# Performance work log

Hardware: AMD Instinct MI355X
Metric: run time of the kernel (lower is better)

Reference implementation:

```python
import jax, jax.numpy as jnp
import numpy as np

N = 100000
E = 1600000
D_IN = 128
D_OUT = 128
HEADS = 4
C = D_OUT // HEADS  # per-head channels = 32
NEG_SLOPE = 0.2
EPS_SOFTMAX = 1e-16
EPS_LN = 1e-5


def setup_inputs() -> dict:
    key = jax.random.key(0)
    ks = jax.random.split(key, 10)
    x = jax.random.normal(ks[0], (N, D_IN), dtype=jnp.float32)
    edge_index = jax.random.randint(ks[1], (2, E), 0, N, dtype=jnp.int64)
    s = 1.0 / np.sqrt(D_IN)
    W = jax.random.normal(ks[2], (D_IN, HEADS * C), dtype=jnp.float32) * s
    att_src = jax.random.normal(ks[3], (HEADS, C), dtype=jnp.float32) * (1.0 / np.sqrt(C))
    att_dst = jax.random.normal(ks[4], (HEADS, C), dtype=jnp.float32) * (1.0 / np.sqrt(C))
    gat_bias = jax.random.normal(ks[5], (D_OUT,), dtype=jnp.float32) * 0.02
    skip_W = jax.random.normal(ks[6], (D_IN, D_OUT), dtype=jnp.float32) * s
    skip_b = jax.random.normal(ks[7], (D_OUT,), dtype=jnp.float32) * 0.02
    ln_g = jnp.ones((D_OUT,), dtype=jnp.float32)
    ln_b = jnp.zeros((D_OUT,), dtype=jnp.float32)
    return {"x": x, "edge_index": edge_index, "W": W, "att_src": att_src,
            "att_dst": att_dst, "gat_bias": gat_bias, "skip_W": skip_W,
            "skip_b": skip_b, "ln_g": ln_g, "ln_b": ln_b}


def _gat_edge_conv(x, src, dst, W, att_src, att_dst, gat_bias, skip_W, skip_b, ln_g, ln_b):
    n = x.shape[0]
    h = (x @ W).reshape(n, HEADS, C)                      # [N,H,C]
    a_s = jnp.einsum('nhc,hc->nh', h, att_src)            # [N,H]
    a_d = jnp.einsum('nhc,hc->nh', h, att_dst)            # [N,H]
    e = jax.nn.leaky_relu(a_s[src] + a_d[dst], NEG_SLOPE)  # [E,H]
    # segment softmax over incoming edges of each dst node
    m = jax.ops.segment_max(e, dst, num_segments=n)        # [N,H]
    p = jnp.exp(e - m[dst])
    z = jax.ops.segment_sum(p, dst, num_segments=n)        # [N,H]
    alpha = p / (z[dst] + EPS_SOFTMAX)                     # [E,H]
    msg = h[src] * alpha[:, :, None]                       # [E,H,C]
    out = jax.ops.segment_sum(msg, dst, num_segments=n)    # [N,H,C]
    out = out.reshape(n, HEADS * C) + gat_bias
    out = out + x @ skip_W + skip_b
    mu = out.mean(-1, keepdims=True)
    var = ((out - mu) ** 2).mean(-1, keepdims=True)
    return (out - mu) * jax.lax.rsqrt(var + EPS_LN) * ln_g + ln_b


def reference(x, edge_index, W, att_src, att_dst, gat_bias, skip_W, skip_b, ln_g, ln_b):
    n = x.shape[0]
    loops = jnp.arange(n, dtype=edge_index.dtype)          # PyG GATConv add_self_loops=True
    src = jnp.concatenate([edge_index[0], loops])
    dst = jnp.concatenate([edge_index[1], loops])
    return _gat_edge_conv(x, src, dst, W, att_src, att_dst, gat_bias, skip_W, skip_b, ln_g, ln_b)
```

## Files before the change

### kernel.cpp

```cpp
#include <hip/hip_runtime.h>
#include <hip/hip_bf16.h>

#define D 128
#define HEADS 4
#define NEG_SLOPE 0.2f
#define QSCALE 0.0625f
#define QUNSCALE 16.0f

#define BCAP64 1280
#define NB_HIST 1600
#define BEPT 16
#define BCHUNK (256 * BEPT)
#define WPREP_BLOCKS 128
#define LDSPAD 136

typedef __attribute__((ext_vector_type(8))) short short8;
typedef __attribute__((ext_vector_type(4))) float f32x4;
typedef __attribute__((ext_vector_type(2))) float f32x2;
typedef __attribute__((ext_vector_type(2))) _Float16 h2;

__device__ __forceinline__ float lrelu(float v) {
    return fmaxf(v, NEG_SLOPE * v);
}

__device__ __forceinline__ short f2bf(float v) {
    __hip_bfloat16 b = __float2bfloat16(v);
    short s;
    __builtin_memcpy(&s, &b, 2);
    return s;
}

__device__ __forceinline__ unsigned short f2h(float v) {
    _Float16 h = (_Float16)v;
    unsigned short s;
    __builtin_memcpy(&s, &h, 2);
    return s;
}

__global__ __launch_bounds__(256)
void prep_kernel(const float* __restrict__ W, const float* __restrict__ S,
                 short* __restrict__ wsT,
                 const int* __restrict__ ei, int* __restrict__ woffA,
                 unsigned int* __restrict__ pairs, int E_, int nb64, int BA) {
    const int t = threadIdx.x;
    if ((int)blockIdx.x >= BA) {
        const int idx = (blockIdx.x - BA) * 256 + t;
        const int nn = idx >> 7, k = idx & 127;
        const float v = (nn < 128) ? W[k * D + nn] : S[k * D + (nn - 128)];
        wsT[idx] = f2bf(v);
        return;
    }
    __shared__ int hist[NB_HIST];
    __shared__ int gbase[NB_HIST];
    for (int q = t; q < nb64; q += 256) hist[q] = 0;
    __syncthreads();
    int sv[BEPT], dv[BEPT], rk[BEPT];
    const int base = blockIdx.x * BCHUNK;
    #pragma unroll
    for (int i = 0; i < BEPT; ++i) {
        const int e = base + i * 256 + t;
        if (e < E_) {
            sv[i] = ei[e];
            dv[i] = ei[E_ + e];
            rk[i] = atomicAdd(&hist[dv[i] >> 6], 1);
        } else {
            sv[i] = -1;
        }
    }
    __syncthreads();
    for (int q = t; q < nb64; q += 256) {
        const int v = hist[q];
        gbase[q] = v ? (q * BCAP64 + atomicAdd(&woffA[q], v)) : 0;
    }
    __syncthreads();
    #pragma unroll
    for (int i = 0; i < BEPT; ++i) {
        if (sv[i] >= 0) {
            const int q = dv[i] >> 6;
            const unsigned int pos = (unsigned int)(gbase[q] + rk[i]);
            if (pos < (unsigned int)(q + 1) * BCAP64)
                pairs[pos] = ((unsigned int)sv[i] << 6) | (unsigned int)(dv[i] & 63);
        }
    }
}

__global__ __launch_bounds__(512, 4)
void mid_kernel(const float* __restrict__ x, const short* __restrict__ wsT,
                const float* __restrict__ skip_b, const float* __restrict__ gat_bias,
                const float* __restrict__ att_src, const float* __restrict__ att_dst,
                unsigned short* __restrict__ hb, unsigned short* __restrict__ baseb,
                float* __restrict__ a_s, float* __restrict__ a_d,
                const unsigned int* __restrict__ pairs, const int* __restrict__ wcur,
                int* __restrict__ cnt, int* __restrict__ offs, int* __restrict__ ssrc,
                int n, int nb64, int nbbB) {
    __shared__ __align__(16) char smem[64 * LDSPAD * 2];
    const int t = threadIdx.x;
    if ((int)blockIdx.x < nbbB) {
        int* lds = (int*)smem;
        const int sub = t >> 8, tt = t & 255;
        int* nh = lds + sub * 160;
        int* sc = lds + sub * 160 + 80;
        const int qb = blockIdx.x * 2 + sub;
        const bool valid = qb < nb64;
        const int sbeg = valid ? qb * BCAP64 : 0;
        int total = valid ? wcur[qb] : 0;
        if (total > BCAP64) total = BCAP64;
        const int send = sbeg + total;
        if (tt < 64) nh[tt] = 0;
        __syncthreads();
        unsigned int pk[6];
        int rk[6];
        int nl = 0;
        #pragma unroll
        for (int r = 0; r < 5; ++r) {
            const int e = sbeg + r * 256 + tt;
            if (e < send) {
                const unsigned int p = pairs[e];
                const int rr = atomicAdd(&nh[p & 63], 1);
                pk[nl] = p; rk[nl] = rr; ++nl;
            }
        }
        __syncthreads();
        const int v = (tt < 64) ? nh[tt] : 0;
        if (tt < 64) sc[tt] = v;
        __syncthreads();
        for (int off = 1; off < 64; off <<= 1) {
            const int xv = (tt >= off && tt < 64) ? sc[tt - off] : 0;
            __syncthreads();
            if (tt < 64) sc[tt] += xv;
            __syncthreads();
        }
        const int ex = (tt < 64) ? sc[tt] - v : 0;
        if (tt < 64 && valid) {
            const int node = qb * 64 + tt;
            if (node < n) { cnt[node] = v; offs[node] = sbeg + ex; }
        }
        __syncthreads();
        if (tt < 64) nh[tt] = ex;
        __syncthreads();
        for (int i = 0; i < nl; ++i)
            ssrc[sbeg + nh[pk[i] & 63] + rk[i]] = (int)(pk[i] >> 6);
        return;
    }
    short (*xs)[LDSPAD] = (short(*)[LDSPAD])smem;
    const int row0 = (blockIdx.x - nbbB) * 64;
    #pragma unroll
    for (int i = 0; i < 4; ++i) {
        const int f = t + 512 * i;
        const int row = f >> 5, c4 = (f & 31) * 4;
        float4 v = make_float4(0.f, 0.f, 0.f, 0.f);
        if (row0 + row < n) v = *(const float4*)&x[(size_t)(row0 + row) * D + c4];
        short4 s4;
        s4.x = f2bf(v.x); s4.y = f2bf(v.y); s4.z = f2bf(v.z); s4.w = f2bf(v.w);
        *(short4*)&xs[row][c4] = s4;
    }
    __syncthreads();
    const int wv = t >> 6, lane = t & 63;
    const int lo = lane & 15, hi = lane >> 4;
    const int wr = wv >> 2;
    const int wc = wv & 3;
    f32x4 acc[2][4] = {};
    #pragma unroll
    for (int k0 = 0; k0 < 128; k0 += 32) {
        const int kk = k0 + hi * 8;
        short8 a0 = *(const short8*)&xs[wr * 32 + lo][kk];
        short8 a1 = *(const short8*)&xs[wr * 32 + 16 + lo][kk];
        #pragma unroll
        for (int nt = 0; nt < 4; ++nt) {
            short8 b = *(const short8*)&wsT[(wc * 64 + nt * 16 + lo) * D + kk];
            acc[0][nt] = __builtin_amdgcn_mfma_f32_16x16x32_bf16(a0, b, acc[0][nt], 0, 0, 0);
            acc[1][nt] = __builtin_amdgcn_mfma_f32_16x16x32_bf16(a1, b, acc[1][nt], 0, 0, 0);
        }
    }
    if (wc < 2) {
        float as_[4], ad_[4];
        #pragma unroll
        for (int nt = 0; nt < 4; ++nt) {
            const int c = wc * 64 + nt * 16 + lo;
            as_[nt] = att_src[c];
            ad_[nt] = att_dst[c];
        }
        #pragma unroll
        for (int mt = 0; mt < 2; ++mt) {
            #pragma unroll
            for (int reg = 0; reg < 4; ++reg) {
                float ps0 = acc[mt][0][reg] * as_[0] + acc[mt][1][reg] * as_[1];
                float ps1 = acc[mt][2][reg] * as_[2] + acc[mt][3][reg] * as_[3];
                float pd0 = acc[mt][0][reg] * ad_[0] + acc[mt][1][reg] * ad_[1];
                float pd1 = acc[mt][2][reg] * ad_[2] + acc[mt][3][reg] * ad_[3];
                #pragma unroll
                for (int off = 1; off < 16; off <<= 1) {
                    ps0 += __shfl_xor(ps0, off, 64);
                    ps1 += __shfl_xor(ps1, off, 64);
                    pd0 += __shfl_xor(pd0, off, 64);
                    pd1 += __shfl_xor(pd1, off, 64);
                }
                if (lo == 0) {
                    const int r = row0 + wr * 32 + mt * 16 + hi * 4 + reg;
                    if (r < n) {
                        a_s[r * HEADS + wc * 2 + 0] = ps0;
                        a_s[r * HEADS + wc * 2 + 1] = ps1;
                        a_d[r * HEADS + wc * 2 + 0] = pd0;
                        a_d[r * HEADS + wc * 2 + 1] = pd1;
                    }
                }
            }
        }
    }
    #pragma unroll
    for (int nt = 0; nt < 4; ++nt) {
        const int cc = wc * 64 + nt * 16 + lo;
        const bool isH = cc < 128;
        const float bb = isH ? 0.f : (skip_b[cc - 128] + gat_bias[cc - 128]);
        unsigned short* dst = isH ? hb : baseb;
        const int c = isH ? cc : cc - 128;
        #pragma unroll
        for (int mt = 0; mt < 2; ++mt) {
            const int rbase = row0 + wr * 32 + mt * 16 + hi * 4;
            #pragma unroll
            for (int reg = 0; reg < 4; ++reg) {
                const int r = rbase + reg;
                if (r < n) dst[(size_t)r * D + c] = f2h(acc[mt][nt][reg] + bb);
            }
        }
    }
}

__global__ __launch_bounds__(256)
void gather_kernel(const int* __restrict__ offs, const int* __restrict__ cnt,
                   const int* __restrict__ ssrc, const float* __restrict__ a_s,
                   const float* __restrict__ a_d, const uint4* __restrict__ hb16,
                   const uint4* __restrict__ baseb16,
                   const float* __restrict__ ln_g, const float* __restrict__ ln_b,
                   float* __restrict__ out, int n) {
    const int lane = threadIdx.x & 63;
    const int i = blockIdx.x * 4 + (threadIdx.x >> 6);
    if (i >= n) return;
    const int e4 = lane >> 2, h4 = lane & 3;
    const int l15 = lane & 15;
    const int grp = lane >> 4;
    const int hh = l15 >> 2;
    const uint4 bv = baseb16[(size_t)i * 16 + l15];
    const float2 g2 = ((const float2*)ln_g)[l15 * 4 + grp];
    const float2 lb2 = ((const float2*)ln_b)[l15 * 4 + grp];
    const float as_h4 = a_s[i * HEADS + h4];
    const float ad_h4 = a_d[i * HEADS + h4];
    const float qself = __expf(lrelu(as_h4 + ad_h4));
    float zacc = (e4 == 0) ? qself : 0.f;
    h2 acc0 = {0.f, 0.f}, acc1 = {0.f, 0.f}, acc2 = {0.f, 0.f}, acc3 = {0.f, 0.f};
    {
        const float qs = __shfl(qself, hh, 64) * QSCALE;
        if (grp == 0) {
            const uint4 u = hb16[(size_t)i * 16 + l15];
            const _Float16 wh = (_Float16)qs;
            const h2 w2 = {wh, wh};
            acc0 = __builtin_bit_cast(h2, u.x) * w2;
            acc1 = __builtin_bit_cast(h2, u.y) * w2;
            acc2 = __builtin_bit_cast(h2, u.z) * w2;
            acc3 = __builtin_bit_cast(h2, u.w) * w2;
        }
    }
    const int o = offs[i];
    const int c = cnt[i];
    for (int k0 = 0; k0 < c; k0 += 16) {
        const int rem = c - k0;
        int srow = 0;
        float q = 0.f;
        if (e4 < rem) {
            const int sidx = ssrc[o + k0 + e4];
            srow = sidx << 4;
            q = __expf(lrelu(a_s[sidx * HEADS + h4] + ad_h4));
        }
        zacc += q;
        const _Float16 qh = (_Float16)(q * QSCALE);
        const h2 qv = {qh, qh};
        const int qpk = __builtin_bit_cast(int, qv);
        const int m = rem < 16 ? rem : 16;
        int ee = 0;
        for (; ee + 8 <= m; ee += 8) {
            const int slA = (ee + grp) << 2;
            const int slB = (ee + 4 + grp) << 2;
            const int rA = __shfl(srow, slA, 64) + l15;
            const int rB = __shfl(srow, slB, 64) + l15;
            const h2 qA = __builtin_bit_cast(h2, __shfl(qpk, slA + hh, 64));
            const h2 qB = __builtin_bit_cast(h2, __shfl(qpk, slB + hh, 64));
            const uint4 uA = hb16[(size_t)(unsigned)rA];
            const uint4 uB = hb16[(size_t)(unsigned)rB];
            acc0 += __builtin_bit_cast(h2, uA.x) * qA;
            acc1 += __builtin_bit_cast(h2, uA.y) * qA;
            acc2 += __builtin_bit_cast(h2, uA.z) * qA;
            acc3 += __builtin_bit_cast(h2, uA.w) * qA;
            acc0 += __builtin_bit_cast(h2, uB.x) * qB;
            acc1 += __builtin_bit_cast(h2, uB.y) * qB;
            acc2 += __builtin_bit_cast(h2, uB.z) * qB;
            acc3 += __builtin_bit_cast(h2, uB.w) * qB;
        }
        for (; ee < m; ee += 4) {
            const int slot = ee + grp;
            const int sl = slot << 2;
            const int rA = __shfl(srow, sl, 64) + l15;
            const h2 qA = __builtin_bit_cast(h2, __shfl(qpk, sl + hh, 64));
            if (slot < m) {
                const uint4 uA = hb16[(size_t)(unsigned)rA];
                acc0 += __builtin_bit_cast(h2, uA.x) * qA;
                acc1 += __builtin_bit_cast(h2, uA.y) * qA;
                acc2 += __builtin_bit_cast(h2, uA.z) * qA;
                acc3 += __builtin_bit_cast(h2, uA.w) * qA;
            }
        }
    }
    #pragma unroll
    for (int off = 16; off < 64; off <<= 1) {
        acc0 += __builtin_bit_cast(h2, __shfl_xor(__builtin_bit_cast(int, acc0), off, 64));
        acc1 += __builtin_bit_cast(h2, __shfl_xor(__builtin_bit_cast(int, acc1), off, 64));
        acc2 += __builtin_bit_cast(h2, __shfl_xor(__builtin_bit_cast(int, acc2), off, 64));
        acc3 += __builtin_bit_cast(h2, __shfl_xor(__builtin_bit_cast(int, acc3), off, 64));
    }
    #pragma unroll
    for (int off = 4; off < 64; off <<= 1) zacc += __shfl_xor(zacc, off, 64);
    const float zz = __shfl(zacc, hh, 64);
    const float rz = QUNSCALE / (zz + 1e-16f);
    const h2 b0 = __builtin_bit_cast(h2, bv.x);
    const h2 b1 = __builtin_bit_cast(h2, bv.y);
    const h2 b2 = __builtin_bit_cast(h2, bv.z);
    const h2 b3 = __builtin_bit_cast(h2, bv.w);
    const float v0 = (float)acc0.x * rz + (float)b0.x;
    const float v1 = (float)acc0.y * rz + (float)b0.y;
    const float v2 = (float)acc1.x * rz + (float)b1.x;
    const float v3 = (float)acc1.y * rz + (float)b1.y;
    const float v4 = (float)acc2.x * rz + (float)b2.x;
    const float v5 = (float)acc2.y * rz + (float)b2.y;
    const float v6 = (float)acc3.x * rz + (float)b3.x;
    const float v7 = (float)acc3.y * rz + (float)b3.y;
    float s1 = v0 + v1 + v2 + v3 + v4 + v5 + v6 + v7;
    float s2 = v0 * v0 + v1 * v1 + v2 * v2 + v3 * v3
             + v4 * v4 + v5 * v5 + v6 * v6 + v7 * v7;
    #pragma unroll
    for (int off = 1; off < 16; off <<= 1) {
        s1 += __shfl_xor(s1, off, 64);
        s2 += __shfl_xor(s2, off, 64);
    }
    const float mu = s1 * (1.f / 128.f);
    const float var = s2 * (1.f / 128.f) - mu * mu;
    const float r = rsqrtf(var + 1e-5f);
    const float lo = grp == 0 ? v0 : grp == 1 ? v2 : grp == 2 ? v4 : v6;
    const float hi = grp == 0 ? v1 : grp == 1 ? v3 : grp == 2 ? v5 : v7;
    f32x2 o2;
    o2.x = (lo - mu) * r * g2.x + lb2.x;
    o2.y = (hi - mu) * r * g2.y + lb2.y;
    __builtin_nontemporal_store(o2, (f32x2*)out + ((size_t)i * 64 + l15 * 4 + grp));
}

extern "C" void kernel_launch(void* const* d_in, const int* in_sizes, int n_in,
                              void* d_out, int out_size, void* d_ws, size_t ws_size,
                              hipStream_t stream) {
    const float* x        = (const float*)d_in[0];
    const int*   ei       = (const int*)d_in[1];
    const float* W        = (const float*)d_in[2];
    const float* att_src  = (const float*)d_in[3];
    const float* att_dst  = (const float*)d_in[4];
    const float* gat_bias = (const float*)d_in[5];
    const float* skip_W   = (const float*)d_in[6];
    const float* skip_b   = (const float*)d_in[7];
    const float* ln_g     = (const float*)d_in[8];
    const float* ln_b     = (const float*)d_in[9];
    float* out = (float*)d_out;

    const int n    = in_sizes[0] / D;
    const int E_   = in_sizes[1] / 2;
    const int nb64 = (n + 63) >> 6;
    const int nbbB = (nb64 + 1) >> 1;

    char* p = (char*)d_ws;
    auto carve = [&p](size_t bytes) {
        char* r = p;
        p += (bytes + 255) & ~(size_t)255;
        return r;
    };
    short* wsT            = (short*)carve(32768 * sizeof(short));
    unsigned short* hb    = (unsigned short*)carve((size_t)n * D * 2);
    unsigned short* baseb = (unsigned short*)carve((size_t)n * D * 2);
    float* a_s            = (float*)carve((size_t)n * HEADS * 4);
    float* a_d            = (float*)carve((size_t)n * HEADS * 4);
    int*   cnt            = (int*)carve((size_t)n * 4);
    int*   offs           = (int*)carve((size_t)n * 4);
    int*   woffA          = (int*)carve((size_t)nb64 * 4);
    int*   ssrc           = (int*)carve((size_t)nb64 * BCAP64 * 4);
    unsigned int* pairs   = (unsigned int*)carve((size_t)nb64 * BCAP64 * 4);

    hipMemsetAsync(woffA, 0, (size_t)nb64 * 4, stream);

    const int BA = (E_ + BCHUNK - 1) / BCHUNK;
    prep_kernel<<<BA + WPREP_BLOCKS, 256, 0, stream>>>(W, skip_W, wsT, ei, woffA,
                                                       pairs, E_, nb64, BA);
    const int ngemm = (n + 63) / 64;
    mid_kernel<<<nbbB + ngemm, 512, 0, stream>>>(x, wsT, skip_b, gat_bias,
                                                 att_src, att_dst,
                                                 hb, baseb, a_s, a_d,
                                                 pairs, woffA,
                                                 cnt, offs, ssrc, n, nb64, nbbB);
    gather_kernel<<<(n + 3) / 4, 256, 0, stream>>>(offs, cnt, ssrc, a_s, a_d,
                                                   (const uint4*)hb,
                                                   (const uint4*)baseb,
                                                   ln_g, ln_b, out, n);
}
```

Before: 270.7 us.

## Regroup stages: fuse edge binning with GEMM, split local sort, vectorize epilogue

Restructures the kernel pipeline. The weight-transpose kernel now also zeroes the bin counters, which replaces a memset. The first edge-binning pass now runs in the same launch as the x@[W|skip_W] GEMM, so binning overlaps with matrix work, and the per-bucket local sort moves into its own kernel. The MFMA operands are swapped so each lane holds 4 consecutive columns of one row, which lets the attention dot products use float4 loads with fewer shuffles and the h/base outputs be written as short4 stores. The cost is an extra launch, and the 512-thread binning blocks must fit their 2x1600-int histograms in the GEMM's LDS buffer.

```diff
diff --git a/kernel.cpp b/kernel.cpp
--- a/kernel.cpp
+++ b/kernel.cpp
@@ -9,9 +9,7 @@
 
 #define BCAP64 1280
 #define NB_HIST 1600
-#define BEPT 16
-#define BCHUNK (256 * BEPT)
-#define WPREP_BLOCKS 128
+#define BCHUNK 4096
 #define LDSPAD 136
 
 typedef __attribute__((ext_vector_type(8))) short short8;
@@ -38,112 +36,63 @@
 }
 
 __global__ __launch_bounds__(256)
-void prep_kernel(const float* __restrict__ W, const float* __restrict__ S,
-                 short* __restrict__ wsT,
-                 const int* __restrict__ ei, int* __restrict__ woffA,
-                 unsigned int* __restrict__ pairs, int E_, int nb64, int BA) {
-    const int t = threadIdx.x;
-    if ((int)blockIdx.x >= BA) {
-        const int idx = (blockIdx.x - BA) * 256 + t;
-        const int nn = idx >> 7, k = idx & 127;
-        const float v = (nn < 128) ? W[k * D + nn] : S[k * D + (nn - 128)];
-        wsT[idx] = f2bf(v);
-        return;
-    }
-    __shared__ int hist[NB_HIST];
-    __shared__ int gbase[NB_HIST];
-    for (int q = t; q < nb64; q += 256) hist[q] = 0;
-    __syncthreads();
-    int sv[BEPT], dv[BEPT], rk[BEPT];
-    const int base = blockIdx.x * BCHUNK;
-    #pragma unroll
-    for (int i = 0; i < BEPT; ++i) {
-        const int e = base + i * 256 + t;
-        if (e < E_) {
-            sv[i] = ei[e];
-            dv[i] = ei[E_ + e];
-            rk[i] = atomicAdd(&hist[dv[i] >> 6], 1);
-        } else {
-            sv[i] = -1;
-        }
-    }
-    __syncthreads();
-    for (int q = t; q < nb64; q += 256) {
-        const int v = hist[q];
-        gbase[q] = v ? (q * BCAP64 + atomicAdd(&woffA[q], v)) : 0;
-    }
-    __syncthreads();
-    #pragma unroll
-    for (int i = 0; i < BEPT; ++i) {
-        if (sv[i] >= 0) {
-            const int q = dv[i] >> 6;
-            const unsigned int pos = (unsigned int)(gbase[q] + rk[i]);
-            if (pos < (unsigned int)(q + 1) * BCAP64)
-                pairs[pos] = ((unsigned int)sv[i] << 6) | (unsigned int)(dv[i] & 63);
-        }
-    }
+void wprep_kernel(const float* __restrict__ W, const float* __restrict__ S,
+                  short* __restrict__ wsT, int* __restrict__ woffA, int nb64) {
+    const int idx = blockIdx.x * 256 + threadIdx.x;
+    const int nn = idx >> 7, k = idx & 127;
+    const float v = (nn < 128) ? W[k * D + nn] : S[k * D + (nn - 128)];
+    wsT[idx] = f2bf(v);
+    if (idx < nb64) woffA[idx] = 0;
 }
 
 __global__ __launch_bounds__(512, 4)
-void mid_kernel(const float* __restrict__ x, const short* __restrict__ wsT,
+void big_kernel(const float* __restrict__ x, const short* __restrict__ wsT,
                 const float* __restrict__ skip_b, const float* __restrict__ gat_bias,
                 const float* __restrict__ att_src, const float* __restrict__ att_dst,
                 unsigned short* __restrict__ hb, unsigned short* __restrict__ baseb,
                 float* __restrict__ a_s, float* __restrict__ a_d,
-                const unsigned int* __restrict__ pairs, const int* __restrict__ wcur,
-                int* __restrict__ cnt, int* __restrict__ offs, int* __restrict__ ssrc,
-                int n, int nb64, int nbbB) {
+                const int* __restrict__ ei, int* __restrict__ woffA,
+                unsigned int* __restrict__ pairs,
+                int n, int E_, int nb64, int BA) {
     __shared__ __align__(16) char smem[64 * LDSPAD * 2];
     const int t = threadIdx.x;
-    if ((int)blockIdx.x < nbbB) {
-        int* lds = (int*)smem;
-        const int sub = t >> 8, tt = t & 255;
-        int* nh = lds + sub * 160;
-        int* sc = lds + sub * 160 + 80;
-        const int qb = blockIdx.x * 2 + sub;
-        const bool valid = qb < nb64;
-        const int sbeg = valid ? qb * BCAP64 : 0;
-        int total = valid ? wcur[qb] : 0;
-        if (total > BCAP64) total = BCAP64;
-        const int send = sbeg + total;
-        if (tt < 64) nh[tt] = 0;
+    if ((int)blockIdx.x < BA) {
+        int* hist = (int*)smem;
+        int* gbase = hist + NB_HIST;
+        for (int q = t; q < nb64; q += 512) hist[q] = 0;
         __syncthreads();
-        unsigned int pk[6];
-        int rk[6];
-        int nl = 0;
-        #pragma unroll
-        for (int r = 0; r < 5; ++r) {
-            const int e = sbeg + r * 256 + tt;
-            if (e < send) {
-                const unsigned int p = pairs[e];
-                const int rr = atomicAdd(&nh[p & 63], 1);
-                pk[nl] = p; rk[nl] = rr; ++nl;
+        int sv[8], dv[8], rk[8];
+        const int base = blockIdx.x * BCHUNK;
+        #pragma unroll
+        for (int i = 0; i < 8; ++i) {
+            const int e = base + i * 512 + t;
+            if (e < E_) {
+                sv[i] = ei[e];
+                dv[i] = ei[E_ + e];
+                rk[i] = atomicAdd(&hist[dv[i] >> 6], 1);
+            } else {
+                sv[i] = -1;
             }
         }
         __syncthreads();
-        const int v = (tt < 64) ? nh[tt] : 0;
-        if (tt < 64) sc[tt] = v;
+        for (int q = t; q < nb64; q += 512) {
+            const int v = hist[q];
+            gbase[q] = v ? (q * BCAP64 + atomicAdd(&woffA[q], v)) : 0;
+        }
         __syncthreads();
-        for (int off = 1; off < 64; off <<= 1) {
-            const int xv = (tt >= off && tt < 64) ? sc[tt - off] : 0;
-            __syncthreads();
-            if (tt < 64) sc[tt] += xv;
-            __syncthreads();
-        }
-        const int ex = (tt < 64) ? sc[tt] - v : 0;
-        if (tt < 64 && valid) {
-            const int node = qb * 64 + tt;
-            if (node < n) { cnt[node] = v; offs[node] = sbeg + ex; }
-        }
-        __syncthreads();
-        if (tt < 64) nh[tt] = ex;
-        __syncthreads();
-        for (int i = 0; i < nl; ++i)
-            ssrc[sbeg + nh[pk[i] & 63] + rk[i]] = (int)(pk[i] >> 6);
+        #pragma unroll
+        for (int i = 0; i < 8; ++i) {
+            if (sv[i] >= 0) {
+                const int q = dv[i] >> 6;
+                const unsigned int pos = (unsigned int)(gbase[q] + rk[i]);
+                if (pos < (unsigned int)(q + 1) * BCAP64)
+                    pairs[pos] = ((unsigned int)sv[i] << 6) | (unsigned int)(dv[i] & 63);
+            }
+        }
         return;
     }
     short (*xs)[LDSPAD] = (short(*)[LDSPAD])smem;
-    const int row0 = (blockIdx.x - nbbB) * 64;
+    const int row0 = (blockIdx.x - BA) * 64;
     #pragma unroll
     for (int i = 0; i < 4; ++i) {
         const int f = t + 512 * i;
@@ -168,62 +117,127 @@
         #pragma unroll
         for (int nt = 0; nt < 4; ++nt) {
             short8 b = *(const short8*)&wsT[(wc * 64 + nt * 16 + lo) * D + kk];
-            acc[0][nt] = __builtin_amdgcn_mfma_f32_16x16x32_bf16(a0, b, acc[0][nt], 0, 0, 0);
-            acc[1][nt] = __builtin_amdgcn_mfma_f32_16x16x32_bf16(a1, b, acc[1][nt], 0, 0, 0);
+            acc[0][nt] = __builtin_amdgcn_mfma_f32_16x16x32_bf16(b, a0, acc[0][nt], 0, 0, 0);
+            acc[1][nt] = __builtin_amdgcn_mfma_f32_16x16x32_bf16(b, a1, acc[1][nt], 0, 0, 0);
         }
     }
     if (wc < 2) {
-        float as_[4], ad_[4];
+        float4 av[4], dv4[4];
         #pragma unroll
         for (int nt = 0; nt < 4; ++nt) {
-            const int c = wc * 64 + nt * 16 + lo;
-            as_[nt] = att_src[c];
-            ad_[nt] = att_dst[c];
+            const int c0 = wc * 64 + nt * 16 + hi * 4;
+            av[nt] = *(const float4*)&att_src[c0];
+            dv4[nt] = *(const float4*)&att_dst[c0];
         }
         #pragma unroll
         for (int mt = 0; mt < 2; ++mt) {
-            #pragma unroll
-            for (int reg = 0; reg < 4; ++reg) {
-                float ps0 = acc[mt][0][reg] * as_[0] + acc[mt][1][reg] * as_[1];
-                float ps1 = acc[mt][2][reg] * as_[2] + acc[mt][3][reg] * as_[3];
-                float pd0 = acc[mt][0][reg] * ad_[0] + acc[mt][1][reg] * ad_[1];
-                float pd1 = acc[mt][2][reg] * ad_[2] + acc[mt][3][reg] * ad_[3];
-                #pragma unroll
-                for (int off = 1; off < 16; off <<= 1) {
-                    ps0 += __shfl_xor(ps0, off, 64);
-                    ps1 += __shfl_xor(ps1, off, 64);
-                    pd0 += __shfl_xor(pd0, off, 64);
-                    pd1 += __shfl_xor(pd1, off, 64);
-                }
-                if (lo == 0) {
-                    const int r = row0 + wr * 32 + mt * 16 + hi * 4 + reg;
-                    if (r < n) {
-                        a_s[r * HEADS + wc * 2 + 0] = ps0;
-                        a_s[r * HEADS + wc * 2 + 1] = ps1;
-                        a_d[r * HEADS + wc * 2 + 0] = pd0;
-                        a_d[r * HEADS + wc * 2 + 1] = pd1;
-                    }
+            float ps0 = acc[mt][0][0] * av[0].x + acc[mt][0][1] * av[0].y
+                      + acc[mt][0][2] * av[0].z + acc[mt][0][3] * av[0].w
+                      + acc[mt][1][0] * av[1].x + acc[mt][1][1] * av[1].y
+                      + acc[mt][1][2] * av[1].z + acc[mt][1][3] * av[1].w;
+            float ps1 = acc[mt][2][0] * av[2].x + acc[mt][2][1] * av[2].y
+                      + acc[mt][2][2] * av[2].z + acc[mt][2][3] * av[2].w
+                      + acc[mt][3][0] * av[3].x + acc[mt][3][1] * av[3].y
+                      + acc[mt][3][2] * av[3].z + acc[mt][3][3] * av[3].w;
+            float pd0 = acc[mt][0][0] * dv4[0].x + acc[mt][0][1] * dv4[0].y
+                      + acc[mt][0][2] * dv4[0].z + acc[mt][0][3] * dv4[0].w
+                      + acc[mt][1][0] * dv4[1].x + acc[mt][1][1] * dv4[1].y
+                      + acc[mt][1][2] * dv4[1].z + acc[mt][1][3] * dv4[1].w;
+            float pd1 = acc[mt][2][0] * dv4[2].x + acc[mt][2][1] * dv4[2].y
+                      + acc[mt][2][2] * dv4[2].z + acc[mt][2][3] * dv4[2].w
+                      + acc[mt][3][0] * dv4[3].x + acc[mt][3][1] * dv4[3].y
+                      + acc[mt][3][2] * dv4[3].z + acc[mt][3][3] * dv4[3].w;
+            ps0 += __shfl_xor(ps0, 16, 64); ps0 += __shfl_xor(ps0, 32, 64);
+            ps1 += __shfl_xor(ps1, 16, 64); ps1 += __shfl_xor(ps1, 32, 64);
+            pd0 += __shfl_xor(pd0, 16, 64); pd0 += __shfl_xor(pd0, 32, 64);
+            pd1 += __shfl_xor(pd1, 16, 64); pd1 += __shfl_xor(pd1, 32, 64);
+            if (lane < 16) {
+                const int r = row0 + wr * 32 + mt * 16 + lane;
+                if (r < n) {
+                    a_s[r * HEADS + wc * 2 + 0] = ps0;
+                    a_s[r * HEADS + wc * 2 + 1] = ps1;
+                    a_d[r * HEADS + wc * 2 + 0] = pd0;
+                    a_d[r * HEADS + wc * 2 + 1] = pd1;
                 }
             }
         }
     }
     #pragma unroll
-    for (int nt = 0; nt < 4; ++nt) {
-        const int cc = wc * 64 + nt * 16 + lo;
-        const bool isH = cc < 128;
-        const float bb = isH ? 0.f : (skip_b[cc - 128] + gat_bias[cc - 128]);
-        unsigned short* dst = isH ? hb : baseb;
-        const int c = isH ? cc : cc - 128;
-        #pragma unroll
-        for (int mt = 0; mt < 2; ++mt) {
-            const int rbase = row0 + wr * 32 + mt * 16 + hi * 4;
-            #pragma unroll
-            for (int reg = 0; reg < 4; ++reg) {
-                const int r = rbase + reg;
-                if (r < n) dst[(size_t)r * D + c] = f2h(acc[mt][nt][reg] + bb);
+    for (int mt = 0; mt < 2; ++mt) {
+        const int r = row0 + wr * 32 + mt * 16 + lo;
+        if (r >= n) continue;
+        #pragma unroll
+        for (int nt = 0; nt < 4; ++nt) {
+            const int cc0 = wc * 64 + nt * 16 + hi * 4;
+            const bool isH = cc0 < 128;
+            const int c0 = isH ? cc0 : cc0 - 128;
+            float4 bb = make_float4(0.f, 0.f, 0.f, 0.f);
+            if (!isH) {
+                const float4 sb = *(const float4*)&skip_b[c0];
+                const float4 gb = *(const float4*)&gat_bias[c0];
+                bb.x = sb.x + gb.x; bb.y = sb.y + gb.y;
+                bb.z = sb.z + gb.z; bb.w = sb.w + gb.w;
             }
-        }
-    }
+            unsigned short* dst = isH ? hb : baseb;
+            short4 s4;
+            s4.x = f2h(acc[mt][nt][0] + bb.x);
+            s4.y = f2h(acc[mt][nt][1] + bb.y);
+            s4.z = f2h(acc[mt][nt][2] + bb.z);
+            s4.w = f2h(acc[mt][nt][3] + bb.w);
+            *(short4*)&dst[(size_t)r * D + c0] = s4;
+        }
+    }
+}
+
+__global__ __launch_bounds__(512)
+void binB_kernel(const unsigned int* __restrict__ pairs, const int* __restrict__ wcur,
+                 int* __restrict__ cnt, int* __restrict__ offs,
+                 int* __restrict__ ssrc, int n, int nb64) {
+    __shared__ int lds[320];
+    const int t = threadIdx.x;
+    const int sub = t >> 8, tt = t & 255;
+    int* nh = lds + sub * 160;
+    int* sc = lds + sub * 160 + 80;
+    const int qb = blockIdx.x * 2 + sub;
+    const bool valid = qb < nb64;
+    const int sbeg = valid ? qb * BCAP64 : 0;
+    int total = valid ? wcur[qb] : 0;
+    if (total > BCAP64) total = BCAP64;
+    const int send = sbeg + total;
+    if (tt < 64) nh[tt] = 0;
+    __syncthreads();
+    unsigned int pk[6];
+    int rk[6];
+    int nl = 0;
+    #pragma unroll
+    for (int r = 0; r < 5; ++r) {
+        const int e = sbeg + r * 256 + tt;
+        if (e < send) {
+            const unsigned int p = pairs[e];
+            const int rr = atomicAdd(&nh[p & 63], 1);
+            pk[nl] = p; rk[nl] = rr; ++nl;
+        }
+    }
+    __syncthreads();
+    const int v = (tt < 64) ? nh[tt] : 0;
+    if (tt < 64) sc[tt] = v;
+    __syncthreads();
+    for (int off = 1; off < 64; off <<= 1) {
+        const int xv = (tt >= off && tt < 64) ? sc[tt - off] : 0;
+        __syncthreads();
+        if (tt < 64) sc[tt] += xv;
+        __syncthreads();
+    }
+    const int ex = (tt < 64) ? sc[tt] - v : 0;
+    if (tt < 64 && valid) {
+        const int node = qb * 64 + tt;
+        if (node < n) { cnt[node] = v; offs[node] = sbeg + ex; }
+    }
+    __syncthreads();
+    if (tt < 64) nh[tt] = ex;
+    __syncthreads();
+    for (int i = 0; i < nl; ++i)
+        ssrc[sbeg + nh[pk[i] & 63] + rk[i]] = (int)(pk[i] >> 6);
 }
 
 __global__ __launch_bounds__(256)
@@ -388,17 +402,15 @@
     int*   ssrc           = (int*)carve((size_t)nb64 * BCAP64 * 4);
     unsigned int* pairs   = (unsigned int*)carve((size_t)nb64 * BCAP64 * 4);
 
-    hipMemsetAsync(woffA, 0, (size_t)nb64 * 4, stream);
-
+    wprep_kernel<<<128, 256, 0, stream>>>(W, skip_W, wsT, woffA, nb64);
     const int BA = (E_ + BCHUNK - 1) / BCHUNK;
-    prep_kernel<<<BA + WPREP_BLOCKS, 256, 0, stream>>>(W, skip_W, wsT, ei, woffA,
-                                                       pairs, E_, nb64, BA);
     const int ngemm = (n + 63) / 64;
-    mid_kernel<<<nbbB + ngemm, 512, 0, stream>>>(x, wsT, skip_b, gat_bias,
-                                                 att_src, att_dst,
-                                                 hb, baseb, a_s, a_d,
-                                                 pairs, woffA,
-                                                 cnt, offs, ssrc, n, nb64, nbbB);
+    big_kernel<<<BA + ngemm, 512, 0, stream>>>(x, wsT, skip_b, gat_bias,
+                                               att_src, att_dst,
+                                               hb, baseb, a_s, a_d,
+                                               ei, woffA, pairs,
+                                               n, E_, nb64, BA);
+    binB_kernel<<<nbbB, 512, 0, stream>>>(pairs, woffA, cnt, offs, ssrc, n, nb64);
     gather_kernel<<<(n + 3) / 4, 256, 0, stream>>>(offs, cnt, ssrc, a_s, a_d,
                                                    (const uint4*)hb,
                                                    (const uint4*)baseb,
```

Measured after the change: 273.0 us. No clear change (+0.8%).
